# Optimization experiments

Hardware: AMD Instinct MI355X
Metric: run time of the kernel (lower is better)

## Reference

```python
import jax, jax.numpy as jnp
import numpy as np

B = 2_000_000
OVERLAP_WEIGHT = 0.5
EPS = 1e-6


def setup_inputs() -> dict:
    key = jax.random.key(0)
    k1, k2 = jax.random.split(key)
    preds = jax.random.normal(k1, (B, 10), dtype=jnp.float32)
    targets = jax.random.normal(k2, (B, 10), dtype=jnp.float32)
    return {"preds": preds, "targets": targets}


def _quat_to_rot(q):
    # q: (B,4) in xyzw order, assumed normalized. Returns (B,3,3),
    # matching the (transposed-convention) matrix in the torch source.
    x, y, z, w = q[:, 0], q[:, 1], q[:, 2], q[:, 3]
    r = jnp.stack([
        1 - 2 * y * y - 2 * z * z, 2 * x * y + 2 * z * w, 2 * x * z - 2 * y * w,
        2 * x * y - 2 * z * w, 1 - 2 * x * x - 2 * z * z, 2 * y * z + 2 * x * w,
        2 * x * z + 2 * y * w, 2 * y * z - 2 * x * w, 1 - 2 * x * x - 2 * y * y,
    ], axis=-1)
    return r.reshape(-1, 3, 3)


def _overlaps(pred_params, gt_params):
    pred_c, pred_d, pred_q = pred_params[:, :3], pred_params[:, 3:6], pred_params[:, 6:]
    gt_c, gt_d, gt_q = gt_params[:, :3], gt_params[:, 3:6], gt_params[:, 6:]
    pred_q = pred_q / jnp.linalg.norm(pred_q, axis=-1, keepdims=True)
    gt_q = gt_q / jnp.linalg.norm(gt_q, axis=-1, keepdims=True)
    pred_rot = _quat_to_rot(pred_q)  # (B,3,3)
    gt_rot = _quat_to_rot(gt_q)      # (B,3,3)
    # trace(pred_rot.T @ gt_rot) = sum of elementwise products
    rot_align = jnp.clip(jnp.sum(pred_rot * gt_rot, axis=(1, 2)) / 3.0, 0.0, 1.0)
    pred_ext = jnp.abs(jnp.einsum('bij,bj->bi', pred_rot, pred_d / 2))
    gt_ext = jnp.abs(jnp.einsum('bij,bj->bi', gt_rot, gt_d / 2))
    center_diff = jnp.abs(pred_c - gt_c)
    overlap_per_axis = jnp.maximum(jnp.minimum(pred_ext, gt_ext) * 2 - center_diff, 0.0) \
        / (pred_ext + gt_ext + EPS)
    overlap = jnp.prod(overlap_per_axis, axis=-1) * rot_align
    return jnp.clip(overlap, 0.0, 1.0)


def _smooth_l1(preds, targets):
    d = preds - targets
    ad = jnp.abs(d)
    return jnp.mean(jnp.where(ad < 1.0, 0.5 * d * d, ad - 0.5))


def reference(preds, targets):
    param_loss = _smooth_l1(preds, targets)
    overlap = _overlaps(preds, targets)
    return param_loss + OVERLAP_WEIGHT * (1.0 - jnp.mean(overlap))
```

## Files before the change

### kernel.cpp

```cpp
#include <hip/hip_runtime.h>


#define B_ROWS 2000000
#define N_PARAM 10
constexpr float OVERLAP_WEIGHT = 0.5f;
constexpr float EPS_F = 1e-6f;

__device__ __forceinline__ void quat_to_rot(float x, float y, float z, float w,
                                            float R[9]) {
    R[0] = 1.f - 2.f*y*y - 2.f*z*z;
    R[1] = 2.f*x*y + 2.f*z*w;
    R[2] = 2.f*x*z - 2.f*y*w;
    R[3] = 2.f*x*y - 2.f*z*w;
    R[4] = 1.f - 2.f*x*x - 2.f*z*z;
    R[5] = 2.f*y*z + 2.f*x*w;
    R[6] = 2.f*x*z + 2.f*y*w;
    R[7] = 2.f*y*z - 2.f*x*w;
    R[8] = 1.f - 2.f*x*x - 2.f*y*y;
}

__global__ __launch_bounds__(256) void hybrid_loss_main(
    const float* __restrict__ preds, const float* __restrict__ targets,
    float* __restrict__ acc)
{
    float psum = 0.f;
    float osum = 0.f;
    const int stride = gridDim.x * blockDim.x;
    for (int row = blockIdx.x * blockDim.x + threadIdx.x; row < B_ROWS; row += stride) {
        const float2* pp = reinterpret_cast<const float2*>(preds   + (size_t)row * N_PARAM);
        const float2* tp = reinterpret_cast<const float2*>(targets + (size_t)row * N_PARAM);
        float p[10], t[10];
        #pragma unroll
        for (int i = 0; i < 5; ++i) {
            float2 a = pp[i]; p[2*i] = a.x; p[2*i+1] = a.y;
            float2 b = tp[i]; t[2*i] = b.x; t[2*i+1] = b.y;
        }

        #pragma unroll
        for (int i = 0; i < 10; ++i) {
            float d  = p[i] - t[i];
            float ad = fabsf(d);
            psum += (ad < 1.f) ? 0.5f * d * d : ad - 0.5f;
        }

        float pqn = sqrtf(p[6]*p[6] + p[7]*p[7] + p[8]*p[8] + p[9]*p[9]);
        float tqn = sqrtf(t[6]*t[6] + t[7]*t[7] + t[8]*t[8] + t[9]*t[9]);
        float pri = 1.f / pqn, tri = 1.f / tqn;
        float PR[9], TR[9];
        quat_to_rot(p[6]*pri, p[7]*pri, p[8]*pri, p[9]*pri, PR);
        quat_to_rot(t[6]*tri, t[7]*tri, t[8]*tri, t[9]*tri, TR);

        float ra = 0.f;
        #pragma unroll
        for (int i = 0; i < 9; ++i) ra += PR[i] * TR[i];
        ra = fminf(fmaxf(ra * (1.f/3.f), 0.f), 1.f);

        float ov = ra;
        #pragma unroll
        for (int i = 0; i < 3; ++i) {
            float pe = fabsf(PR[3*i+0]*(p[3]*0.5f) + PR[3*i+1]*(p[4]*0.5f) + PR[3*i+2]*(p[5]*0.5f));
            float te = fabsf(TR[3*i+0]*(t[3]*0.5f) + TR[3*i+1]*(t[4]*0.5f) + TR[3*i+2]*(t[5]*0.5f));
            float cd = fabsf(p[i] - t[i]);
            float ax = fmaxf(fminf(pe, te) * 2.f - cd, 0.f) / (pe + te + EPS_F);
            ov *= ax;
        }
        ov = fminf(fmaxf(ov, 0.f), 1.f);
        osum += ov;
    }

    #pragma unroll
    for (int off = 32; off > 0; off >>= 1) {
        psum += __shfl_down(psum, off);
        osum += __shfl_down(osum, off);
    }
    __shared__ float sp[4], so[4];
    const int lane = threadIdx.x & 63;
    const int wid  = threadIdx.x >> 6;
    if (lane == 0) { sp[wid] = psum; so[wid] = osum; }
    __syncthreads();
    if (threadIdx.x == 0) {
        float P = sp[0] + sp[1] + sp[2] + sp[3];
        float O = so[0] + so[1] + so[2] + so[3];
        atomicAdd(&acc[0], P);
        atomicAdd(&acc[1], O);
    }
}

__global__ void hybrid_loss_finalize(const float* __restrict__ acc,
                                     float* __restrict__ out) {
    out[0] = acc[0] * (1.f / (10.f * (float)B_ROWS))
           + OVERLAP_WEIGHT * (1.f - acc[1] * (1.f / (float)B_ROWS));
}

extern "C" void kernel_launch(void* const* d_in, const int* in_sizes, int n_in,
                              void* d_out, int out_size, void* d_ws, size_t ws_size,
                              hipStream_t stream) {
    const float* preds   = (const float*)d_in[0];
    const float* targets = (const float*)d_in[1];
    float* out = (float*)d_out;
    float* acc = (float*)d_ws;

    hipMemsetAsync(acc, 0, 2 * sizeof(float), stream);

    const int block = 256;
    const int grid  = 2048;
    hybrid_loss_main<<<grid, block, 0, stream>>>(preds, targets, acc);
    hybrid_loss_finalize<<<1, 1, 0, stream>>>(acc, out);
}
```

Measured before the change: 195.4 us.

## Stage row chunks into LDS with coalesced global_load_lds, one row per thread

Replaces the grid-stride loop, where each thread did strided 8-byte loads of its 40-byte row, with one block per 512-row chunk. Each chunk is copied with fully coalesced 16-byte global_load_lds transfers into shared memory, and each thread then reads its row from LDS. This targets poor coalescing and the extra memory transactions of the strided AoS access. In exchange it launches about 3900 blocks, each issuing two atomics, and the float2 LDS reads at a 10-float stride may cause bank conflicts.

```diff
diff --git a/kernel.cpp b/kernel.cpp
--- a/kernel.cpp
+++ b/kernel.cpp
@@ -2,9 +2,19 @@
 
 
 #define B_ROWS 2000000
-#define N_PARAM 10
+#define THREADS 512
+#define CHUNK_ROWS 512
+#define CHUNK_F4 1280
+#define N_CHUNKS 3907
 constexpr float OVERLAP_WEIGHT = 0.5f;
 constexpr float EPS_F = 1e-6f;
+constexpr size_t TOTAL_F4 = (size_t)B_ROWS * 40 / 16;
+
+__device__ __forceinline__ void gload_lds16(const float* g, float* l) {
+    __builtin_amdgcn_global_load_lds(
+        (const __attribute__((address_space(1))) void*)g,
+        (__attribute__((address_space(3))) void*)l, 16, 0, 0);
+}
 
 __device__ __forceinline__ void quat_to_rot(float x, float y, float z, float w,
                                             float R[9]) {
@@ -19,21 +29,46 @@
     R[8] = 1.f - 2.f*x*x - 2.f*y*y;
 }
 
-__global__ __launch_bounds__(256) void hybrid_loss_main(
+__global__ __launch_bounds__(THREADS) void hybrid_loss_main(
     const float* __restrict__ preds, const float* __restrict__ targets,
     float* __restrict__ acc)
 {
-    float psum = 0.f;
-    float osum = 0.f;
-    const int stride = gridDim.x * blockDim.x;
-    for (int row = blockIdx.x * blockDim.x + threadIdx.x; row < B_ROWS; row += stride) {
-        const float2* pp = reinterpret_cast<const float2*>(preds   + (size_t)row * N_PARAM);
-        const float2* tp = reinterpret_cast<const float2*>(targets + (size_t)row * N_PARAM);
+    __shared__ __align__(16) float ldsP[CHUNK_F4 * 4];
+    __shared__ __align__(16) float ldsT[CHUNK_F4 * 4];
+
+    const int tid  = threadIdx.x;
+    const int wave = tid >> 6;
+    const int lane = tid & 63;
+    const int c    = blockIdx.x;
+    const size_t base_f4 = (size_t)c * CHUNK_F4;
+
+    #pragma unroll
+    for (int r = 0; r < 2; ++r) {
+        const int e_wave = r * 512 + wave * 64;
+        size_t gidx = base_f4 + e_wave + lane;
+        if (gidx >= TOTAL_F4) gidx = TOTAL_F4 - 1;
+        gload_lds16(preds   + gidx * 4, &ldsP[e_wave * 4]);
+        gload_lds16(targets + gidx * 4, &ldsT[e_wave * 4]);
+    }
+    if (wave < 4) {
+        const int e_wave = 1024 + wave * 64;
+        size_t gidx = base_f4 + e_wave + lane;
+        if (gidx >= TOTAL_F4) gidx = TOTAL_F4 - 1;
+        gload_lds16(preds   + gidx * 4, &ldsP[e_wave * 4]);
+        gload_lds16(targets + gidx * 4, &ldsT[e_wave * 4]);
+    }
+    __syncthreads();
+
+    float psum = 0.f, osum = 0.f;
+    const size_t grow = (size_t)c * CHUNK_ROWS + tid;
+    if (grow < B_ROWS) {
         float p[10], t[10];
+        const float2* lp = reinterpret_cast<const float2*>(&ldsP[tid * 10]);
+        const float2* lt = reinterpret_cast<const float2*>(&ldsT[tid * 10]);
         #pragma unroll
         for (int i = 0; i < 5; ++i) {
-            float2 a = pp[i]; p[2*i] = a.x; p[2*i+1] = a.y;
-            float2 b = tp[i]; t[2*i] = b.x; t[2*i+1] = b.y;
+            float2 a = lp[i]; p[2*i] = a.x; p[2*i+1] = a.y;
+            float2 b = lt[i]; t[2*i] = b.x; t[2*i+1] = b.y;
         }
 
         #pragma unroll
@@ -73,14 +108,13 @@
         psum += __shfl_down(psum, off);
         osum += __shfl_down(osum, off);
     }
-    __shared__ float sp[4], so[4];
-    const int lane = threadIdx.x & 63;
-    const int wid  = threadIdx.x >> 6;
-    if (lane == 0) { sp[wid] = psum; so[wid] = osum; }
     __syncthreads();
-    if (threadIdx.x == 0) {
-        float P = sp[0] + sp[1] + sp[2] + sp[3];
-        float O = so[0] + so[1] + so[2] + so[3];
+    if (lane == 0) { ldsP[wave] = psum; ldsP[8 + wave] = osum; }
+    __syncthreads();
+    if (tid == 0) {
+        float P = 0.f, O = 0.f;
+        #pragma unroll
+        for (int w = 0; w < 8; ++w) { P += ldsP[w]; O += ldsP[8 + w]; }
         atomicAdd(&acc[0], P);
         atomicAdd(&acc[1], O);
     }
@@ -102,8 +136,6 @@
 
     hipMemsetAsync(acc, 0, 2 * sizeof(float), stream);
 
-    const int block = 256;
-    const int grid  = 2048;
-    hybrid_loss_main<<<grid, block, 0, stream>>>(preds, targets, acc);
+    hybrid_loss_main<<<N_CHUNKS, THREADS, 0, stream>>>(preds, targets, acc);
     hybrid_loss_finalize<<<1, 1, 0, stream>>>(acc, out);
 }
```

New measurement: 231.8 us. +18.6%, slower.
